# Optimization experiments

Measured on AMD Instinct MI355X. Metric: run time of the kernel, lower is better.

The kernel has to match this reference:

```python
import jax, jax.numpy as jnp
import numpy as np

H = 256      # hidden_size
L = 20       # max_length
V = 29       # output_size (vocab)
LAT = H + 8


def setup_inputs() -> dict:
    key = jax.random.key(0)
    ks = jax.random.split(key, 20)
    s = 0.05
    return {
        "input_tensor": jax.random.randint(ks[0], (1,), 0, V),
        "hidden": jax.random.normal(ks[1], (1, 1, H), dtype=jnp.float32),
        "encoder_outputs": jax.random.normal(ks[2], (L, H), dtype=jnp.float32),
        "cond": jax.random.randint(ks[3], (2,), 0, 4),
        "is_head": 1,
        # parameters (PyTorch Linear convention: weight [out, in])
        "emb": jax.random.normal(ks[4], (V, H), dtype=jnp.float32) * s,
        "w_l2d": jax.random.normal(ks[5], (H, LAT), dtype=jnp.float32) * s,
        "b_l2d": jnp.zeros((H,), dtype=jnp.float32),
        "w_attn": jax.random.normal(ks[6], (L, 2 * H), dtype=jnp.float32) * s,
        "b_attn": jnp.zeros((L,), dtype=jnp.float32),
        "w_comb": jax.random.normal(ks[7], (H, 2 * H), dtype=jnp.float32) * s,
        "b_comb": jnp.zeros((H,), dtype=jnp.float32),
        "w_ih": jax.random.normal(ks[8], (3 * H, H), dtype=jnp.float32) * s,
        "w_hh": jax.random.normal(ks[9], (3 * H, H), dtype=jnp.float32) * s,
        "b_ih": jnp.zeros((3 * H,), dtype=jnp.float32),
        "b_hh": jnp.zeros((3 * H,), dtype=jnp.float32),
        "w_out": jax.random.normal(ks[10], (V, H), dtype=jnp.float32) * s,
        "b_out": jnp.zeros((V,), dtype=jnp.float32),
    }


def gru_cell(x, h, w_ih, w_hh, b_ih, b_hh):
    # x, h: [1, H]; PyTorch GRU gate order: r, z, n
    gi = x @ w_ih.T + b_ih
    gh = h @ w_hh.T + b_hh
    ir, iz, inn = jnp.split(gi, 3, axis=-1)
    hr, hz, hn = jnp.split(gh, 3, axis=-1)
    r = jax.nn.sigmoid(ir + hr)
    z = jax.nn.sigmoid(iz + hz)
    n = jnp.tanh(inn + r * hn)
    return (1.0 - z) * n + z * h


def reference(input_tensor, hidden, encoder_outputs, cond, is_head,
              emb, w_l2d, b_l2d, w_attn, b_attn, w_comb, b_comb,
              w_ih, w_hh, b_ih, b_hh, w_out, b_out):
    if is_head:
        c = jnp.concatenate([jax.nn.one_hot(cond[0], 4),
                             jax.nn.one_hot(cond[1], 4)]).astype(hidden.dtype)  # [8]
        hidden = jnp.concatenate([hidden, c[None, None, :]], axis=2)  # [1,1,H+8]
        hidden = hidden @ w_l2d.T + b_l2d                              # [1,1,H]
    embedded = emb[input_tensor].reshape(1, 1, -1)                     # [1,1,H] (dropout: eval mode)
    attn_in = jnp.concatenate([embedded[0], hidden[0]], axis=1)        # [1,2H]
    attn_weights = jax.nn.softmax(attn_in @ w_attn.T + b_attn, axis=1) # [1,L]
    attn_applied = attn_weights @ encoder_outputs                      # [1,H]
    output = jnp.concatenate([embedded[0], attn_applied], axis=1)      # [1,2H]
    output = jax.nn.relu(output @ w_comb.T + b_comb)                   # [1,H]
    h_new = gru_cell(output, hidden[0], w_ih, w_hh, b_ih, b_hh)        # [1,H]
    logits = jax.nn.log_softmax(h_new @ w_out.T + b_out, axis=1)       # [1,V]
    return logits, h_new[None], attn_weights
```

## Files before the change

### kernel.cpp

```cpp
#include <hip/hip_runtime.h>
#include <hip/hip_bf16.h>

#define H 256
#define L 20
#define V 29
#define LAT 264
#define NBLK 66
#define NTHR 256
#define TOK 0x13370001


__device__ __forceinline__ float wave_sum(float v) {
#pragma unroll
    for (int o = 32; o > 0; o >>= 1) v += __shfl_down(v, o, 64);
    return v;
}

__device__ __forceinline__ float ldws(const float* p) {
    return __hip_atomic_load(p, __ATOMIC_RELAXED, __HIP_MEMORY_SCOPE_AGENT);
}
__device__ __forceinline__ void stws(float* p, float v) {
    __hip_atomic_store(p, v, __ATOMIC_RELAXED, __HIP_MEMORY_SCOPE_AGENT);
}

__device__ __forceinline__ void set_my_flag(int* flags) {
    __syncthreads();
    if (threadIdx.x == 0)
        __hip_atomic_store(&flags[blockIdx.x * 16], TOK,
                           __ATOMIC_RELAXED, __HIP_MEMORY_SCOPE_AGENT);
}

__device__ __forceinline__ void wait_flags(int* flags, int first, int n) {
    const int t = threadIdx.x;
    if (t < n) {
        long spins = 0;
        while (__hip_atomic_load(&flags[(first + t) * 16], __ATOMIC_RELAXED,
                                 __HIP_MEMORY_SCOPE_AGENT) != TOK) {
            __builtin_amdgcn_s_sleep(1);
            if (++spins > 200000000L) break;
        }
    }
    __syncthreads();
}

__device__ __forceinline__ void copy_g2l4(float* dst, const float* src, int nfloats) {
    const float4* s4 = (const float4*)src;
    float4* d4 = (float4*)dst;
    const int n4 = nfloats >> 2;
    for (int i = threadIdx.x; i < n4; i += NTHR) d4[i] = s4[i];
}

__global__ __launch_bounds__(NTHR) void decoder_step(
    const int* inp, const float* hidden, const float* enc,
    const int* cond, const int* is_head,
    const float* emb, const float* w_l2d, const float* b_l2d,
    const float* w_attn, const float* b_attn,
    const float* w_comb, const float* b_comb,
    const float* w_ih, const float* w_hh,
    const float* b_ih, const float* b_hh,
    const float* w_out, const float* b_out,
    float* ws, float* out)
{
    extern __shared__ float sm[];
    const int b = blockIdx.x;
    const int t = threadIdx.x;
    const int wave = t >> 6, lane = t & 63;
    int* flags = (int*)(ws + 2304);

    if (b < 16) {
        float* w   = sm;
        float* xin = sm + 4224;
        float* bl  = sm + 4224 + 264;
        const int row0 = b * 16;
        copy_g2l4(w, w_l2d + row0 * LAT, 16 * LAT);
        xin[t] = hidden[t];
        if (t < 8) {
            int c = (t < 4) ? cond[0] : cond[1];
            int jj = (t < 4) ? t : t - 4;
            xin[H + t] = (c == jj) ? 1.0f : 0.0f;
        }
        if (t < 16) bl[t] = b_l2d[row0 + t];
        __syncthreads();
        if (is_head[0]) {
            for (int r = wave; r < 16; r += 4) {
                float s = 0.f;
#pragma unroll
                for (int j = lane; j < LAT; j += 64) s += w[r * LAT + j] * xin[j];
                s = wave_sum(s);
                if (lane == 0) stws(&ws[row0 + r], s + bl[r]);
            }
        } else {
            if (t < 16) stws(&ws[row0 + t], xin[row0 + t]);
        }
        set_my_flag(flags);

    } else if (b == 16) {
        float* wat  = sm;
        float* encl = sm + 10240;
        float* xatt = sm + 15360;
        float* ba   = sm + 15872;
        float* aw   = sm + 15904;
        float* lg   = sm + 15936;
        copy_g2l4(wat, w_attn, L * 2 * H);
        copy_g2l4(encl, enc, L * H);
        copy_g2l4(xatt, emb + inp[0] * H, H);
        if (t < L) ba[t] = b_attn[t];
        wait_flags(flags, 0, 16);
        xatt[H + t] = ldws(ws + t);
        __syncthreads();
        for (int r = wave; r < L; r += 4) {
            float s = 0.f;
#pragma unroll
            for (int j = lane; j < 2 * H; j += 64) s += wat[r * 2 * H + j] * xatt[j];
            s = wave_sum(s);
            if (lane == 0) lg[r] = s + ba[r];
        }
        __syncthreads();
        if (wave == 0) {
            float v = (lane < L) ? lg[lane] : -1e30f;
            float m = v;
#pragma unroll
            for (int o = 32; o > 0; o >>= 1) m = fmaxf(m, __shfl_xor(m, o, 64));
            float e = (lane < L) ? __expf(v - m) : 0.f;
            float ssum = e;
#pragma unroll
            for (int o = 32; o > 0; o >>= 1) ssum += __shfl_xor(ssum, o, 64);
            if (lane < L) {
                float a = e / ssum;
                aw[lane] = a;
                out[V + H + lane] = a;
            }
        }
        __syncthreads();
        {
            float s = 0.f;
#pragma unroll
            for (int l = 0; l < L; ++l) s += aw[l] * encl[l * H + t];
            stws(&ws[H + t], s);
        }
        set_my_flag(flags);

    } else if (b < 33) {
        float* w  = sm;
        float* x  = sm + 8192;
        float* bc = sm + 8704;
        const int row0 = (b - 17) * 16;
        copy_g2l4(w, w_comb + row0 * 2 * H, 16 * 2 * H);
        copy_g2l4(x, emb + inp[0] * H, H);
        if (t < 16) bc[t] = b_comb[row0 + t];
        wait_flags(flags, 16, 1);
        x[H + t] = ldws(ws + H + t);
        __syncthreads();
        for (int r = wave; r < 16; r += 4) {
            float s = 0.f;
#pragma unroll
            for (int j = lane; j < 2 * H; j += 64) s += w[r * 2 * H + j] * x[j];
            s = wave_sum(s);
            if (lane == 0) stws(&ws[512 + row0 + r], fmaxf(s + bc[r], 0.f));
        }
        set_my_flag(flags);

    } else if (b < 49) {
        float* w  = sm;
        float* x  = sm + 12288;
        float* bb = sm + 12288 + 256;
        const int row0 = (b - 33) * 48;
        copy_g2l4(w, w_ih + row0 * H, 48 * H);
        if (t < 48) bb[t] = b_ih[row0 + t];
        wait_flags(flags, 17, 16);
        x[t] = ldws(ws + 512 + t);
        __syncthreads();
        for (int r = wave; r < 48; r += 4) {
            float s = 0.f;
#pragma unroll
            for (int j = lane; j < H; j += 64) s += w[r * H + j] * x[j];
            s = wave_sum(s);
            if (lane == 0) stws(&ws[768 + row0 + r], s + bb[r]);
        }
        set_my_flag(flags);

    } else if (b < 65) {
        float* w  = sm;
        float* x  = sm + 12288;
        float* bb = sm + 12288 + 256;
        const int row0 = (b - 49) * 48;
        copy_g2l4(w, w_hh + row0 * H, 48 * H);
        if (t < 48) bb[t] = b_hh[row0 + t];
        wait_flags(flags, 0, 16);
        x[t] = ldws(ws + t);
        __syncthreads();
        for (int r = wave; r < 48; r += 4) {
            float s = 0.f;
#pragma unroll
            for (int j = lane; j < H; j += 64) s += w[r * H + j] * x[j];
            s = wave_sum(s);
            if (lane == 0) stws(&ws[1536 + row0 + r], s + bb[r]);
        }
        set_my_flag(flags);

    } else {
        float* w  = sm;
        float* bo = sm + 7424;
        float* hn = sm + 7424 + 32;
        float* lg = sm + 7424 + 32 + 256;
        copy_g2l4(w, w_out, V * H);
        if (t < V) bo[t] = b_out[t];
        wait_flags(flags, 33, 32);
        {
            float gi1 = ldws(ws + 768 + t);
            float gi2 = ldws(ws + 768 + H + t);
            float gi3 = ldws(ws + 768 + 2 * H + t);
            float gh1 = ldws(ws + 1536 + t);
            float gh2 = ldws(ws + 1536 + H + t);
            float gh3 = ldws(ws + 1536 + 2 * H + t);
            float h2  = ldws(ws + t);
            float r = 1.f / (1.f + __expf(-(gi1 + gh1)));
            float z = 1.f / (1.f + __expf(-(gi2 + gh2)));
            float n = tanhf(gi3 + r * gh3);
            float h = (1.f - z) * n + z * h2;
            hn[t] = h;
            out[V + t] = h;
        }
        __syncthreads();
        for (int r = wave; r < V; r += 4) {
            float s = 0.f;
#pragma unroll
            for (int j = lane; j < H; j += 64) s += w[r * H + j] * hn[j];
            s = wave_sum(s);
            if (lane == 0) lg[r] = s + bo[r];
        }
        __syncthreads();
        if (wave == 0) {
            float v = (lane < V) ? lg[lane] : -1e30f;
            float m = v;
#pragma unroll
            for (int o = 32; o > 0; o >>= 1) m = fmaxf(m, __shfl_xor(m, o, 64));
            float e = (lane < V) ? __expf(v - m) : 0.f;
            float s2 = e;
#pragma unroll
            for (int o = 32; o > 0; o >>= 1) s2 += __shfl_xor(s2, o, 64);
            float ls = logf(s2);
            if (lane < V) out[lane] = v - m - ls;
        }
    }
}

extern "C" void kernel_launch(void* const* d_in, const int* in_sizes, int n_in,
                              void* d_out, int out_size, void* d_ws, size_t ws_size,
                              hipStream_t stream) {
    const int* inp      = (const int*)d_in[0];
    const float* hidden = (const float*)d_in[1];
    const float* enc    = (const float*)d_in[2];
    const int* cond     = (const int*)d_in[3];
    const int* is_head  = (const int*)d_in[4];
    const float* emb    = (const float*)d_in[5];
    const float* w_l2d  = (const float*)d_in[6];
    const float* b_l2d  = (const float*)d_in[7];
    const float* w_attn = (const float*)d_in[8];
    const float* b_attn = (const float*)d_in[9];
    const float* w_comb = (const float*)d_in[10];
    const float* b_comb = (const float*)d_in[11];
    const float* w_ih   = (const float*)d_in[12];
    const float* w_hh   = (const float*)d_in[13];
    const float* b_ih   = (const float*)d_in[14];
    const float* b_hh   = (const float*)d_in[15];
    const float* w_out  = (const float*)d_in[16];
    const float* b_out  = (const float*)d_in[17];

    float* ws = (float*)d_ws;
    float* out = (float*)d_out;

    const size_t smem = 15968 * sizeof(float);
    decoder_step<<<NBLK, NTHR, smem, stream>>>(
        inp, hidden, enc, cond, is_head, emb, w_l2d, b_l2d, w_attn, b_attn,
        w_comb, b_comb, w_ih, w_hh, b_ih, b_hh, w_out, b_out, ws, out);
}
```

Before: 104.4 us.

## Fuse attention into combine blocks and GRU gates into gate blocks to cut grid barriers

Each of the 16 combine blocks now computes the attention softmax and weighted sum itself, so the separate attention block and its flag wait go away. The embedding half of the attention logits is computed before waiting on the hidden state. The w_ih and w_hh rows are regrouped per hidden slice so each w_ih block applies the GRU nonlinearity for its own 16 columns, and the output block only waits on those blocks. The gain is fewer dependent inter-block hops, paid for with attention work repeated 16 times and uncached global reads of w_attn and enc.

```diff
diff --git a/kernel.cpp b/kernel.cpp
--- a/kernel.cpp
+++ b/kernel.cpp
@@ -5,7 +5,7 @@
 #define L 20
 #define V 29
 #define LAT 264
-#define NBLK 66
+#define NBLK 65
 #define NTHR 256
 #define TOK 0x13370001
 
@@ -94,26 +94,39 @@
         }
         set_my_flag(flags);
 
-    } else if (b == 16) {
-        float* wat  = sm;
-        float* encl = sm + 10240;
-        float* xatt = sm + 15360;
-        float* ba   = sm + 15872;
-        float* aw   = sm + 15904;
-        float* lg   = sm + 15936;
-        copy_g2l4(wat, w_attn, L * 2 * H);
-        copy_g2l4(encl, enc, L * H);
-        copy_g2l4(xatt, emb + inp[0] * H, H);
-        if (t < L) ba[t] = b_attn[t];
+    } else if (b < 32) {
+        float* wah = sm;
+        float* wc  = sm + 5120;
+        float* xin = sm + 5120 + 8192;
+        float* lge = xin + 512;
+        float* lg  = lge + 32;
+        float* aw  = lg + 32;
+        float* bc  = aw + 32;
+        const int k = b - 16, row0 = k * 16;
+        for (int i = t; i < L * 64; i += NTHR) {
+            int r = i >> 6, q = i & 63;
+            ((float4*)wah)[r * 64 + q] = ((const float4*)(w_attn + r * 2 * H + H))[q];
+        }
+        copy_g2l4(wc, w_comb + row0 * 2 * H, 16 * 2 * H);
+        xin[t] = emb[inp[0] * H + t];
+        if (t < 16) bc[t] = b_comb[row0 + t];
+        __syncthreads();
+        for (int r = wave; r < L; r += 4) {
+            float s = 0.f;
+#pragma unroll
+            for (int j = lane; j < H; j += 64) s += w_attn[r * 2 * H + j] * xin[j];
+            s = wave_sum(s);
+            if (lane == 0) lge[r] = s + b_attn[r];
+        }
         wait_flags(flags, 0, 16);
-        xatt[H + t] = ldws(ws + t);
+        xin[H + t] = ldws(ws + t);
         __syncthreads();
         for (int r = wave; r < L; r += 4) {
             float s = 0.f;
 #pragma unroll
-            for (int j = lane; j < 2 * H; j += 64) s += wat[r * 2 * H + j] * xatt[j];
-            s = wave_sum(s);
-            if (lane == 0) lg[r] = s + ba[r];
+            for (int j = lane; j < H; j += 64) s += wah[r * H + j] * xin[H + j];
+            s = wave_sum(s);
+            if (lane == 0) lg[r] = lge[r] + s;
         }
         __syncthreads();
         if (wave == 0) {
@@ -128,99 +141,98 @@
             if (lane < L) {
                 float a = e / ssum;
                 aw[lane] = a;
-                out[V + H + lane] = a;
+                if (b == 16) out[V + H + lane] = a;
             }
         }
         __syncthreads();
         {
             float s = 0.f;
 #pragma unroll
-            for (int l = 0; l < L; ++l) s += aw[l] * encl[l * H + t];
-            stws(&ws[H + t], s);
-        }
-        set_my_flag(flags);
-
-    } else if (b < 33) {
-        float* w  = sm;
-        float* x  = sm + 8192;
-        float* bc = sm + 8704;
-        const int row0 = (b - 17) * 16;
-        copy_g2l4(w, w_comb + row0 * 2 * H, 16 * 2 * H);
-        copy_g2l4(x, emb + inp[0] * H, H);
-        if (t < 16) bc[t] = b_comb[row0 + t];
-        wait_flags(flags, 16, 1);
-        x[H + t] = ldws(ws + H + t);
+            for (int l = 0; l < L; ++l) s += aw[l] * enc[l * H + t];
+            xin[H + t] = s;
+        }
         __syncthreads();
         for (int r = wave; r < 16; r += 4) {
             float s = 0.f;
 #pragma unroll
-            for (int j = lane; j < 2 * H; j += 64) s += w[r * 2 * H + j] * x[j];
+            for (int j = lane; j < 2 * H; j += 64) s += wc[r * 2 * H + j] * xin[j];
             s = wave_sum(s);
             if (lane == 0) stws(&ws[512 + row0 + r], fmaxf(s + bc[r], 0.f));
         }
         set_my_flag(flags);
 
-    } else if (b < 49) {
+    } else if (b < 48) {
+        float* w   = sm;
+        float* x   = sm + 12288;
+        float* bb  = x + 256;
+        float* gis = bb + 48;
+        const int k = b - 32, c0 = k * 16;
+        copy_g2l4(w,             w_ih + c0 * H,            16 * H);
+        copy_g2l4(w + 16 * H,    w_ih + (H + c0) * H,      16 * H);
+        copy_g2l4(w + 32 * H,    w_ih + (2 * H + c0) * H,  16 * H);
+        if (t < 48) {
+            int g = t >> 4, i = t & 15;
+            bb[t] = b_ih[g * H + c0 + i];
+        }
+        wait_flags(flags, 16, 16);
+        x[t] = ldws(ws + 512 + t);
+        __syncthreads();
+        for (int m = wave; m < 48; m += 4) {
+            float s = 0.f;
+#pragma unroll
+            for (int j = lane; j < H; j += 64) s += w[m * H + j] * x[j];
+            s = wave_sum(s);
+            if (lane == 0) gis[m] = s + bb[m];
+        }
+        wait_flags(flags, 48 + k, 1);
+        if (t < 16) {
+            const float* ghp = ws + 1536 + k * 48;
+            float ghr = ldws(ghp + t);
+            float ghz = ldws(ghp + 16 + t);
+            float ghn = ldws(ghp + 32 + t);
+            float h2  = ldws(ws + c0 + t);
+            float r = 1.f / (1.f + __expf(-(gis[t] + ghr)));
+            float z = 1.f / (1.f + __expf(-(gis[16 + t] + ghz)));
+            float n = tanhf(gis[32 + t] + r * ghn);
+            float h = (1.f - z) * n + z * h2;
+            out[V + c0 + t] = h;
+            stws(&ws[768 + c0 + t], h);
+        }
+        set_my_flag(flags);
+
+    } else if (b < 64) {
         float* w  = sm;
         float* x  = sm + 12288;
-        float* bb = sm + 12288 + 256;
-        const int row0 = (b - 33) * 48;
-        copy_g2l4(w, w_ih + row0 * H, 48 * H);
-        if (t < 48) bb[t] = b_ih[row0 + t];
-        wait_flags(flags, 17, 16);
-        x[t] = ldws(ws + 512 + t);
-        __syncthreads();
-        for (int r = wave; r < 48; r += 4) {
-            float s = 0.f;
-#pragma unroll
-            for (int j = lane; j < H; j += 64) s += w[r * H + j] * x[j];
-            s = wave_sum(s);
-            if (lane == 0) stws(&ws[768 + row0 + r], s + bb[r]);
-        }
-        set_my_flag(flags);
-
-    } else if (b < 65) {
-        float* w  = sm;
-        float* x  = sm + 12288;
-        float* bb = sm + 12288 + 256;
-        const int row0 = (b - 49) * 48;
-        copy_g2l4(w, w_hh + row0 * H, 48 * H);
-        if (t < 48) bb[t] = b_hh[row0 + t];
+        float* bb = x + 256;
+        const int k = b - 48, c0 = k * 16;
+        copy_g2l4(w,             w_hh + c0 * H,            16 * H);
+        copy_g2l4(w + 16 * H,    w_hh + (H + c0) * H,      16 * H);
+        copy_g2l4(w + 32 * H,    w_hh + (2 * H + c0) * H,  16 * H);
+        if (t < 48) {
+            int g = t >> 4, i = t & 15;
+            bb[t] = b_hh[g * H + c0 + i];
+        }
         wait_flags(flags, 0, 16);
         x[t] = ldws(ws + t);
         __syncthreads();
-        for (int r = wave; r < 48; r += 4) {
-            float s = 0.f;
-#pragma unroll
-            for (int j = lane; j < H; j += 64) s += w[r * H + j] * x[j];
-            s = wave_sum(s);
-            if (lane == 0) stws(&ws[1536 + row0 + r], s + bb[r]);
+        for (int m = wave; m < 48; m += 4) {
+            float s = 0.f;
+#pragma unroll
+            for (int j = lane; j < H; j += 64) s += w[m * H + j] * x[j];
+            s = wave_sum(s);
+            if (lane == 0) stws(&ws[1536 + k * 48 + m], s + bb[m]);
         }
         set_my_flag(flags);
 
     } else {
         float* w  = sm;
         float* bo = sm + 7424;
-        float* hn = sm + 7424 + 32;
-        float* lg = sm + 7424 + 32 + 256;
+        float* hn = bo + 32;
+        float* lg = hn + 256;
         copy_g2l4(w, w_out, V * H);
         if (t < V) bo[t] = b_out[t];
-        wait_flags(flags, 33, 32);
-        {
-            float gi1 = ldws(ws + 768 + t);
-            float gi2 = ldws(ws + 768 + H + t);
-            float gi3 = ldws(ws + 768 + 2 * H + t);
-            float gh1 = ldws(ws + 1536 + t);
-            float gh2 = ldws(ws + 1536 + H + t);
-            float gh3 = ldws(ws + 1536 + 2 * H + t);
-            float h2  = ldws(ws + t);
-            float r = 1.f / (1.f + __expf(-(gi1 + gh1)));
-            float z = 1.f / (1.f + __expf(-(gi2 + gh2)));
-            float n = tanhf(gi3 + r * gh3);
-            float h = (1.f - z) * n + z * h2;
-            hn[t] = h;
-            out[V + t] = h;
-        }
+        wait_flags(flags, 32, 16);
+        hn[t] = ldws(ws + 768 + t);
         __syncthreads();
         for (int r = wave; r < V; r += 4) {
             float s = 0.f;
@@ -270,7 +282,7 @@
     float* ws = (float*)d_ws;
     float* out = (float*)d_out;
 
-    const size_t smem = 15968 * sizeof(float);
+    const size_t smem = 14080 * sizeof(float);
     decoder_step<<<NBLK, NTHR, smem, stream>>>(
         inp, hidden, enc, cond, is_head, emb, w_l2d, b_l2d, w_attn, b_attn,
         w_comb, b_comb, w_ih, w_hh, b_ih, b_hh, w_out, b_out, ws, out);
```

Measured after the change: 107.7 us. 1.03x slower.
